# Optimization experiments

Measured on AMD Instinct MI355X. Metric: run time of the kernel, lower is better.

The kernel has to match this reference:

```python
import jax, jax.numpy as jnp
import numpy as np


def setup_inputs() -> dict:
    key = jax.random.key(0)
    kq, kk, kv = jax.random.split(key, 3)
    n, d = 8192, 128
    Q = jax.random.normal(kq, (n, d), dtype=jnp.float32)
    K = jax.random.normal(kk, (n, d), dtype=jnp.float32)
    V = jax.random.normal(kv, (n, d), dtype=jnp.float32)
    return {"Q": Q, "K": K, "V": V}


def reference(Q, K, V):
    # The blockwise online-softmax loops in the torch module compute exactly
    # softmax(Q @ K^T) @ V  -- note: NO 1/sqrt(d) scaling in the original.
    S = jnp.einsum('qd,kd->qk', Q, K)          # [n, n] scores
    P = jax.nn.softmax(S, axis=-1)             # numerically stable softmax
    O = jnp.einsum('qk,kd->qd', P, V)          # [n, d]
    return O
```

## Files before the change

kernel.cpp:

```cpp
#include <hip/hip_runtime.h>
#include <hip/hip_bf16.h>

#define N 8192
#define D 128
#define NSPLIT 8
#define KVSPLIT (N / NSPLIT)
#define KVBLK 64
#define NT (KVSPLIT / KVBLK)
#define L2E 1.442695041f

typedef __attribute__((ext_vector_type(8))) _Float16 half8;
typedef __attribute__((ext_vector_type(2))) __fp16 fp16x2;
typedef __attribute__((ext_vector_type(16))) float f32x16;

union H8 { fp16x2 h2[4]; half8 h8; };

__device__ __forceinline__ float fexp2(float x) {
    float r; asm("v_exp_f32 %0, %1" : "=v"(r) : "v"(x)); return r;
}

__global__ void prep_kernel(const float* __restrict__ Q, const float* __restrict__ K,
                            const float* __restrict__ V, _Float16* __restrict__ Qh,
                            _Float16* __restrict__ Kh, _Float16* __restrict__ Vtp) {
    __shared__ _Float16 tile[64][65];
    const int bid = blockIdx.x;
    const int tid = threadIdx.x;
    if (bid < 1024) {
        const float4* src = (const float4*)(bid < 512 ? Q : K);
        _Float16* dst = (bid < 512) ? Qh : Kh;
        const int b = bid & 511;
#pragma unroll
        for (int p = 0; p < 2; ++p) {
            int i = b * 512 + p * 256 + tid;
            float4 v = src[i];
            ushort4 o;
            o.x = __builtin_bit_cast(ushort, (_Float16)v.x);
            o.y = __builtin_bit_cast(ushort, (_Float16)v.y);
            o.z = __builtin_bit_cast(ushort, (_Float16)v.z);
            o.w = __builtin_bit_cast(ushort, (_Float16)v.w);
            *reinterpret_cast<ushort4*>(dst + (size_t)i * 4) = o;
        }
    } else {
        const int vbid = bid - 1024;
        const int k0 = (vbid & 127) * 64;
        const int d0 = (vbid >> 7) * 64;
#pragma unroll
        for (int p = 0; p < 16; ++p) {
            int flat = p * 256 + tid;
            int r = flat >> 6, cc = flat & 63;
            tile[r][cc] = (_Float16)(V[(size_t)(k0 + r) * D + d0 + cc]);
        }
        __syncthreads();
#pragma unroll
        for (int p = 0; p < 16; ++p) {
            int flat = p * 256 + tid;
            int dd = flat >> 6, kl = flat & 63;
            int kk = kl & 31;
            int s32 = 16 * (kk >> 4) + 8 * ((kk >> 2) & 1) + 4 * ((kk >> 3) & 1) + (kk & 3);
            Vtp[(size_t)(d0 + dd) * N + k0 + (kl & 32) + s32] = tile[kl][dd];
        }
    }
}

#define STAGE(kdst_, vdst_, kbase_)                                                   \
    {                                                                                 \
        _Pragma("unroll")                                                             \
        for (int p = 0; p < 4; ++p) {                                                 \
            int c4 = p * 256 + tid;                                                   \
            int row = c4 >> 4, chs = c4 & 15;                                         \
            int cc = (chs & 8) | ((chs & 7) ^ (row & 7));                             \
            __builtin_amdgcn_global_load_lds(                                         \
                (const __attribute__((address_space(1))) void*)(Kh + (size_t)((kbase_) + row) * D + cc * 8), \
                (__attribute__((address_space(3))) void*)((kdst_) + c4 * 8), 16, 0, 0);              \
        }                                                                             \
        _Pragma("unroll")                                                             \
        for (int p = 0; p < 4; ++p) {                                                 \
            int c4 = p * 256 + tid;                                                   \
            int dd = c4 >> 3, chs = c4 & 7;                                           \
            int cc = chs ^ (dd & 7);                                                  \
            __builtin_amdgcn_global_load_lds(                                         \
                (const __attribute__((address_space(1))) void*)(Vtp + (size_t)dd * N + (kbase_) + cc * 8),   \
                (__attribute__((address_space(3))) void*)((vdst_) + c4 * 8), 16, 0, 0);              \
        }                                                                             \
    }

__launch_bounds__(256, 2)
__global__ void fa_kernel(const _Float16* __restrict__ Qh, const _Float16* __restrict__ Kh,
                          const _Float16* __restrict__ Vtp, _Float16* __restrict__ Oph,
                          float* __restrict__ Mpart, float* __restrict__ Lpart) {
    __shared__ __align__(16) _Float16 smem[32768];

    const int tid  = threadIdx.x;
    const int w    = tid >> 6;
    const int lane = tid & 63;
    const int h    = lane >> 5;
    const int c    = lane & 31;
    const int bid  = blockIdx.x;
    const int split = bid & 7;
    const int bx   = bid >> 3;
    const int q0w  = bx * 128 + w * 32;
    const int kv0  = split * KVSPLIT;

    half8 qa[8];
    {
        const _Float16* qrow = Qh + (size_t)(q0w + c) * D + h * 8;
#pragma unroll
        for (int st = 0; st < 8; ++st)
            qa[st] = *reinterpret_cast<const half8*>(qrow + st * 16);
    }

    f32x16 oacc[4];
#pragma unroll
    for (int dt = 0; dt < 4; ++dt)
#pragma unroll
        for (int r = 0; r < 16; ++r) oacc[dt][r] = 0.f;
    float mrun = -1e30f, lrun = 0.f;
    H8 pk[4];

    STAGE(smem, smem + 16384, kv0);
    __syncthreads();

    for (int t = 0; t < NT; ++t) {
        const int cur = t & 1;
        if (t + 1 < NT)
            STAGE(smem + (cur ^ 1) * 8192, smem + 16384 + (cur ^ 1) * 8192,
                  kv0 + (t + 1) * KVBLK);

        const _Float16* kb = smem + cur * 8192;
        const _Float16* vb = smem + 16384 + cur * 8192;

        half8 kf[16];
#pragma unroll
        for (int st = 0; st < 8; ++st) {
            int ch = st * 2 + h;
            int pos = (ch & 8) | ((ch & 7) ^ (c & 7));
            kf[st]     = *reinterpret_cast<const half8*>(kb + c * 128 + pos * 8);
            kf[8 + st] = *reinterpret_cast<const half8*>(kb + (32 + c) * 128 + pos * 8);
        }

        f32x16 sb0, sb1;
#pragma unroll
        for (int r = 0; r < 16; ++r) { sb0[r] = 0.f; sb1[r] = 0.f; }
        __builtin_amdgcn_s_setprio(1);
#pragma unroll
        for (int st = 0; st < 8; ++st) {
            sb0 = __builtin_amdgcn_mfma_f32_32x32x16_f16(kf[st], qa[st], sb0, 0, 0, 0);
            sb1 = __builtin_amdgcn_mfma_f32_32x32x16_f16(kf[8 + st], qa[st], sb1, 0, 0, 0);
        }
        __builtin_amdgcn_s_setprio(0);

        float mx[16];
#pragma unroll
        for (int r = 0; r < 16; ++r) mx[r] = fmaxf(sb0[r], sb1[r]);
#pragma unroll
        for (int s = 8; s > 0; s >>= 1)
#pragma unroll
            for (int r = 0; r < s; ++r) mx[r] = fmaxf(mx[r], mx[r + s]);
        float pmax = fmaxf(mx[0], __shfl_xor(mx[0], 32));

        if (!__all(pmax <= mrun + 8.0f)) {
            float nm = fmaxf(mrun, pmax);
            float scl = fexp2((mrun - nm) * L2E);
            lrun *= scl;
#pragma unroll
            for (int dt = 0; dt < 4; ++dt)
#pragma unroll
                for (int r = 0; r < 16; ++r) oacc[dt][r] *= scl;
            mrun = nm;
        }
        const float nml = -mrun * L2E;
#pragma unroll
        for (int r = 0; r < 16; ++r) sb0[r] = fexp2(__builtin_fmaf(sb0[r], L2E, nml));
#pragma unroll
        for (int r = 0; r < 16; ++r) sb1[r] = fexp2(__builtin_fmaf(sb1[r], L2E, nml));
        float ts[16];
#pragma unroll
        for (int r = 0; r < 16; ++r) ts[r] = sb0[r] + sb1[r];
#pragma unroll
        for (int s = 8; s > 0; s >>= 1)
#pragma unroll
            for (int r = 0; r < s; ++r) ts[r] += ts[r + s];
        lrun += ts[0] + __shfl_xor(ts[0], 32);

#pragma unroll
        for (int i = 0; i < 4; ++i) {
            pk[0].h2[i] = __builtin_amdgcn_cvt_pkrtz(sb0[2 * i], sb0[2 * i + 1]);
            pk[1].h2[i] = __builtin_amdgcn_cvt_pkrtz(sb0[8 + 2 * i], sb0[8 + 2 * i + 1]);
            pk[2].h2[i] = __builtin_amdgcn_cvt_pkrtz(sb1[2 * i], sb1[2 * i + 1]);
            pk[3].h2[i] = __builtin_amdgcn_cvt_pkrtz(sb1[8 + 2 * i], sb1[8 + 2 * i + 1]);
        }

        half8 vf[16];
#pragma unroll
        for (int j = 0; j < 4; ++j) {
            int ch = j * 2 + h;
#pragma unroll
            for (int dt = 0; dt < 4; ++dt) {
                int dd = dt * 32 + c;
                int pos = ch ^ (dd & 7);
                vf[j * 4 + dt] = *reinterpret_cast<const half8*>(vb + dd * 64 + pos * 8);
            }
        }

        __builtin_amdgcn_s_setprio(1);
#pragma unroll
        for (int j = 0; j < 4; ++j)
#pragma unroll
            for (int dt = 0; dt < 4; ++dt)
                oacc[dt] = __builtin_amdgcn_mfma_f32_32x32x16_f16(vf[j * 4 + dt], pk[j].h8,
                                                                  oacc[dt], 0, 0, 0);
        __builtin_amdgcn_s_setprio(0);

        __syncthreads();
    }

    __syncthreads();
    float inv = 1.0f / lrun;
    float* epi = reinterpret_cast<float*>(smem) + w * 1088;
    const size_t sbase = (size_t)split * N;
#pragma unroll
    for (int dt = 0; dt < 4; ++dt) {
#pragma unroll
        for (int r = 0; r < 16; ++r) {
            int dloc = (r & 3) + 8 * (r >> 2) + 4 * h;
            epi[c * 33 + dloc] = oacc[dt][r] * inv;
        }
#pragma unroll
        for (int it = 0; it < 16; ++it) {
            int j = it * 64 + lane;
            int rr = j >> 5, cc2 = j & 31;
            Oph[(sbase + q0w + rr) * D + dt * 32 + cc2] = (_Float16)epi[rr * 33 + cc2];
        }
    }
    if (h == 0) {
        Mpart[sbase + q0w + c] = mrun;
        Lpart[sbase + q0w + c] = lrun;
    }
}

__global__ void fa_merge(const _Float16* __restrict__ Oph, const float* __restrict__ Mpart,
                         const float* __restrict__ Lpart, float* __restrict__ O) {
    int idx = blockIdx.x * 256 + threadIdx.x;
    int q = idx >> 7;
    int d = idx & 127;
    float m[NSPLIT];
    float M = -1e30f;
#pragma unroll
    for (int s = 0; s < NSPLIT; ++s) {
        m[s] = Mpart[s * N + q];
        M = fmaxf(M, m[s]);
    }
    float acc = 0.f, wsum = 0.f;
#pragma unroll
    for (int s = 0; s < NSPLIT; ++s) {
        float wgt = fexp2((m[s] - M) * L2E) * Lpart[s * N + q];
        acc += wgt * (float)Oph[((size_t)s * N + q) * D + d];
        wsum += wgt;
    }
    O[idx] = acc / wsum;
}

extern "C" void kernel_launch(void* const* d_in, const int* in_sizes, int n_in,
                              void* d_out, int out_size, void* d_ws, size_t ws_size,
                              hipStream_t stream) {
    const float* Q = (const float*)d_in[0];
    const float* K = (const float*)d_in[1];
    const float* V = (const float*)d_in[2];
    float* O = (float*)d_out;

    _Float16* Qh = (_Float16*)d_ws;
    _Float16* Kh = Qh + (size_t)N * D;
    _Float16* Vtp = Kh + (size_t)N * D;
    _Float16* Oph = Vtp + (size_t)N * D;
    float* Mpart = (float*)(Oph + (size_t)NSPLIT * N * D);
    float* Lpart = Mpart + (size_t)NSPLIT * N;

    hipLaunchKernelGGL(prep_kernel, dim3(1280), dim3(256), 0, stream,
                       Q, K, V, Qh, Kh, Vtp);
    hipLaunchKernelGGL(fa_kernel, dim3((N / 128) * NSPLIT), dim3(256), 0, stream,
                       Qh, Kh, Vtp, Oph, Mpart, Lpart);
    hipLaunchKernelGGL(fa_merge, dim3(N * D / 256), dim3(256), 0, stream,
                       Oph, Mpart, Lpart, O);
}
```

Baseline: 60.98 us.

## Process 64 query rows per wave and double KV splits

Each wave now handles two 32-row query tiles that share every K and V fragment read from LDS. This halves LDS traffic per MFMA and halves the KV tile loads per query. To keep the grid the same size, the KV range is split 16 ways instead of 8. The per-key-tile work is also split into two 32-key sub-steps with separate softmax updates. The cost is much higher register pressure (8 output accumulators plus two Q fragment sets), shorter KV loops per block, and twice the partial output written to and merged from workspace.

```diff
diff --git a/kernel.cpp b/kernel.cpp
--- a/kernel.cpp
+++ b/kernel.cpp
@@ -3,7 +3,7 @@
 
 #define N 8192
 #define D 128
-#define NSPLIT 8
+#define NSPLIT 16
 #define KVSPLIT (N / NSPLIT)
 #define KVBLK 64
 #define NT (KVSPLIT / KVBLK)
@@ -84,6 +84,44 @@
         }                                                                             \
     }
 
+#define SOFTMAX_PACK(S_, MR_, LR_, OB_, PK_)                                          \
+    {                                                                                 \
+        float mx[8];                                                                  \
+        _Pragma("unroll")                                                             \
+        for (int r = 0; r < 8; ++r) mx[r] = fmaxf(S_[r], S_[r + 8]);                  \
+        _Pragma("unroll")                                                             \
+        for (int sd = 4; sd > 0; sd >>= 1)                                            \
+            _Pragma("unroll")                                                         \
+            for (int r = 0; r < sd; ++r) mx[r] = fmaxf(mx[r], mx[r + sd]);            \
+        float pmax = fmaxf(mx[0], __shfl_xor(mx[0], 32));                             \
+        if (!__all(pmax <= MR_ + 8.0f)) {                                             \
+            float nm = fmaxf(MR_, pmax);                                              \
+            float scl = fexp2((MR_ - nm) * L2E);                                      \
+            LR_ *= scl;                                                               \
+            _Pragma("unroll")                                                         \
+            for (int dt = 0; dt < 4; ++dt)                                            \
+                _Pragma("unroll")                                                     \
+                for (int r = 0; r < 16; ++r) oacc[(OB_) + dt][r] *= scl;              \
+            MR_ = nm;                                                                 \
+        }                                                                             \
+        const float nml = -MR_ * L2E;                                                 \
+        _Pragma("unroll")                                                             \
+        for (int r = 0; r < 16; ++r) S_[r] = fexp2(__builtin_fmaf(S_[r], L2E, nml));  \
+        float tsum[8];                                                                \
+        _Pragma("unroll")                                                             \
+        for (int r = 0; r < 8; ++r) tsum[r] = S_[r] + S_[r + 8];                      \
+        _Pragma("unroll")                                                             \
+        for (int sd = 4; sd > 0; sd >>= 1)                                            \
+            _Pragma("unroll")                                                         \
+            for (int r = 0; r < sd; ++r) tsum[r] += tsum[r + sd];                     \
+        LR_ += tsum[0] + __shfl_xor(tsum[0], 32);                                     \
+        _Pragma("unroll")                                                             \
+        for (int i = 0; i < 4; ++i) {                                                 \
+            PK_[0].h2[i] = __builtin_amdgcn_cvt_pkrtz(S_[2 * i], S_[2 * i + 1]);      \
+            PK_[1].h2[i] = __builtin_amdgcn_cvt_pkrtz(S_[8 + 2 * i], S_[8 + 2 * i + 1]); \
+        }                                                                             \
+    }
+
 __launch_bounds__(256, 2)
 __global__ void fa_kernel(const _Float16* __restrict__ Qh, const _Float16* __restrict__ Kh,
                           const _Float16* __restrict__ Vtp, _Float16* __restrict__ Oph,
@@ -96,26 +134,28 @@
     const int h    = lane >> 5;
     const int c    = lane & 31;
     const int bid  = blockIdx.x;
-    const int split = bid & 7;
-    const int bx   = bid >> 3;
-    const int q0w  = bx * 128 + w * 32;
+    const int split = bid & (NSPLIT - 1);
+    const int bx   = bid >> 4;
+    const int q0w  = bx * 256 + w * 64;
     const int kv0  = split * KVSPLIT;
 
-    half8 qa[8];
+    half8 qaA[8], qaB[8];
     {
-        const _Float16* qrow = Qh + (size_t)(q0w + c) * D + h * 8;
-#pragma unroll
-        for (int st = 0; st < 8; ++st)
-            qa[st] = *reinterpret_cast<const half8*>(qrow + st * 16);
-    }
-
-    f32x16 oacc[4];
-#pragma unroll
-    for (int dt = 0; dt < 4; ++dt)
-#pragma unroll
-        for (int r = 0; r < 16; ++r) oacc[dt][r] = 0.f;
-    float mrun = -1e30f, lrun = 0.f;
-    H8 pk[4];
+        const _Float16* qrA = Qh + (size_t)(q0w + c) * D + h * 8;
+        const _Float16* qrB = Qh + (size_t)(q0w + 32 + c) * D + h * 8;
+#pragma unroll
+        for (int st = 0; st < 8; ++st) {
+            qaA[st] = *reinterpret_cast<const half8*>(qrA + st * 16);
+            qaB[st] = *reinterpret_cast<const half8*>(qrB + st * 16);
+        }
+    }
+
+    f32x16 oacc[8];
+#pragma unroll
+    for (int i = 0; i < 8; ++i)
+#pragma unroll
+        for (int r = 0; r < 16; ++r) oacc[i][r] = 0.f;
+    float mrunA = -1e30f, lrunA = 0.f, mrunB = -1e30f, lrunB = 0.f;
 
     STAGE(smem, smem + 16384, kv0);
     __syncthreads();
@@ -129,112 +169,87 @@
         const _Float16* kb = smem + cur * 8192;
         const _Float16* vb = smem + 16384 + cur * 8192;
 
-        half8 kf[16];
-#pragma unroll
-        for (int st = 0; st < 8; ++st) {
-            int ch = st * 2 + h;
-            int pos = (ch & 8) | ((ch & 7) ^ (c & 7));
-            kf[st]     = *reinterpret_cast<const half8*>(kb + c * 128 + pos * 8);
-            kf[8 + st] = *reinterpret_cast<const half8*>(kb + (32 + c) * 128 + pos * 8);
-        }
-
-        f32x16 sb0, sb1;
-#pragma unroll
-        for (int r = 0; r < 16; ++r) { sb0[r] = 0.f; sb1[r] = 0.f; }
-        __builtin_amdgcn_s_setprio(1);
-#pragma unroll
-        for (int st = 0; st < 8; ++st) {
-            sb0 = __builtin_amdgcn_mfma_f32_32x32x16_f16(kf[st], qa[st], sb0, 0, 0, 0);
-            sb1 = __builtin_amdgcn_mfma_f32_32x32x16_f16(kf[8 + st], qa[st], sb1, 0, 0, 0);
-        }
-        __builtin_amdgcn_s_setprio(0);
-
-        float mx[16];
-#pragma unroll
-        for (int r = 0; r < 16; ++r) mx[r] = fmaxf(sb0[r], sb1[r]);
-#pragma unroll
-        for (int s = 8; s > 0; s >>= 1)
-#pragma unroll
-            for (int r = 0; r < s; ++r) mx[r] = fmaxf(mx[r], mx[r + s]);
-        float pmax = fmaxf(mx[0], __shfl_xor(mx[0], 32));
-
-        if (!__all(pmax <= mrun + 8.0f)) {
-            float nm = fmaxf(mrun, pmax);
-            float scl = fexp2((mrun - nm) * L2E);
-            lrun *= scl;
-#pragma unroll
-            for (int dt = 0; dt < 4; ++dt)
-#pragma unroll
-                for (int r = 0; r < 16; ++r) oacc[dt][r] *= scl;
-            mrun = nm;
-        }
-        const float nml = -mrun * L2E;
-#pragma unroll
-        for (int r = 0; r < 16; ++r) sb0[r] = fexp2(__builtin_fmaf(sb0[r], L2E, nml));
-#pragma unroll
-        for (int r = 0; r < 16; ++r) sb1[r] = fexp2(__builtin_fmaf(sb1[r], L2E, nml));
-        float ts[16];
-#pragma unroll
-        for (int r = 0; r < 16; ++r) ts[r] = sb0[r] + sb1[r];
-#pragma unroll
-        for (int s = 8; s > 0; s >>= 1)
-#pragma unroll
-            for (int r = 0; r < s; ++r) ts[r] += ts[r + s];
-        lrun += ts[0] + __shfl_xor(ts[0], 32);
-
-#pragma unroll
-        for (int i = 0; i < 4; ++i) {
-            pk[0].h2[i] = __builtin_amdgcn_cvt_pkrtz(sb0[2 * i], sb0[2 * i + 1]);
-            pk[1].h2[i] = __builtin_amdgcn_cvt_pkrtz(sb0[8 + 2 * i], sb0[8 + 2 * i + 1]);
-            pk[2].h2[i] = __builtin_amdgcn_cvt_pkrtz(sb1[2 * i], sb1[2 * i + 1]);
-            pk[3].h2[i] = __builtin_amdgcn_cvt_pkrtz(sb1[8 + 2 * i], sb1[8 + 2 * i + 1]);
-        }
-
-        half8 vf[16];
-#pragma unroll
-        for (int j = 0; j < 4; ++j) {
-            int ch = j * 2 + h;
-#pragma unroll
-            for (int dt = 0; dt < 4; ++dt) {
-                int dd = dt * 32 + c;
-                int pos = ch ^ (dd & 7);
-                vf[j * 4 + dt] = *reinterpret_cast<const half8*>(vb + dd * 64 + pos * 8);
-            }
-        }
-
-        __builtin_amdgcn_s_setprio(1);
-#pragma unroll
-        for (int j = 0; j < 4; ++j)
-#pragma unroll
-            for (int dt = 0; dt < 4; ++dt)
-                oacc[dt] = __builtin_amdgcn_mfma_f32_32x32x16_f16(vf[j * 4 + dt], pk[j].h8,
-                                                                  oacc[dt], 0, 0, 0);
-        __builtin_amdgcn_s_setprio(0);
+#pragma unroll
+        for (int s = 0; s < 2; ++s) {
+            f32x16 sA, sB;
+#pragma unroll
+            for (int r = 0; r < 16; ++r) { sA[r] = 0.f; sB[r] = 0.f; }
+            __builtin_amdgcn_s_setprio(1);
+#pragma unroll
+            for (int st = 0; st < 8; ++st) {
+                int ch = st * 2 + h;
+                int pos = (ch & 8) | ((ch & 7) ^ (c & 7));
+                half8 kf = *reinterpret_cast<const half8*>(kb + (s * 32 + c) * 128 + pos * 8);
+                sA = __builtin_amdgcn_mfma_f32_32x32x16_f16(kf, qaA[st], sA, 0, 0, 0);
+                sB = __builtin_amdgcn_mfma_f32_32x32x16_f16(kf, qaB[st], sB, 0, 0, 0);
+            }
+            __builtin_amdgcn_s_setprio(0);
+
+            H8 pkA[2], pkB[2];
+            SOFTMAX_PACK(sA, mrunA, lrunA, 0, pkA)
+            SOFTMAX_PACK(sB, mrunB, lrunB, 4, pkB)
+
+            __builtin_amdgcn_s_setprio(1);
+#pragma unroll
+            for (int j = 0; j < 2; ++j) {
+                int ch = s * 4 + j * 2 + h;
+#pragma unroll
+                for (int dt = 0; dt < 4; ++dt) {
+                    int dd = dt * 32 + c;
+                    int pos = ch ^ (dd & 7);
+                    half8 vf = *reinterpret_cast<const half8*>(vb + dd * 64 + pos * 8);
+                    oacc[dt]     = __builtin_amdgcn_mfma_f32_32x32x16_f16(vf, pkA[j].h8, oacc[dt], 0, 0, 0);
+                    oacc[4 + dt] = __builtin_amdgcn_mfma_f32_32x32x16_f16(vf, pkB[j].h8, oacc[4 + dt], 0, 0, 0);
+                }
+            }
+            __builtin_amdgcn_s_setprio(0);
+        }
 
         __syncthreads();
     }
 
     __syncthreads();
-    float inv = 1.0f / lrun;
     float* epi = reinterpret_cast<float*>(smem) + w * 1088;
     const size_t sbase = (size_t)split * N;
-#pragma unroll
-    for (int dt = 0; dt < 4; ++dt) {
-#pragma unroll
-        for (int r = 0; r < 16; ++r) {
-            int dloc = (r & 3) + 8 * (r >> 2) + 4 * h;
-            epi[c * 33 + dloc] = oacc[dt][r] * inv;
-        }
-#pragma unroll
-        for (int it = 0; it < 16; ++it) {
-            int j = it * 64 + lane;
-            int rr = j >> 5, cc2 = j & 31;
-            Oph[(sbase + q0w + rr) * D + dt * 32 + cc2] = (_Float16)epi[rr * 33 + cc2];
+    {
+        float inv = 1.0f / lrunA;
+#pragma unroll
+        for (int dt = 0; dt < 4; ++dt) {
+#pragma unroll
+            for (int r = 0; r < 16; ++r) {
+                int dloc = (r & 3) + 8 * (r >> 2) + 4 * h;
+                epi[c * 33 + dloc] = oacc[dt][r] * inv;
+            }
+#pragma unroll
+            for (int it = 0; it < 16; ++it) {
+                int j = it * 64 + lane;
+                int rr = j >> 5, cc2 = j & 31;
+                Oph[(sbase + q0w + rr) * D + dt * 32 + cc2] = (_Float16)epi[rr * 33 + cc2];
+            }
+        }
+    }
+    {
+        float inv = 1.0f / lrunB;
+#pragma unroll
+        for (int dt = 0; dt < 4; ++dt) {
+#pragma unroll
+            for (int r = 0; r < 16; ++r) {
+                int dloc = (r & 3) + 8 * (r >> 2) + 4 * h;
+                epi[c * 33 + dloc] = oacc[4 + dt][r] * inv;
+            }
+#pragma unroll
+            for (int it = 0; it < 16; ++it) {
+                int j = it * 64 + lane;
+                int rr = j >> 5, cc2 = j & 31;
+                Oph[(sbase + q0w + 32 + rr) * D + dt * 32 + cc2] = (_Float16)epi[rr * 33 + cc2];
+            }
         }
     }
     if (h == 0) {
-        Mpart[sbase + q0w + c] = mrun;
-        Lpart[sbase + q0w + c] = lrun;
+        Mpart[sbase + q0w + c] = mrunA;
+        Lpart[sbase + q0w + c] = lrunA;
+        Mpart[sbase + q0w + 32 + c] = mrunB;
+        Lpart[sbase + q0w + 32 + c] = lrunB;
     }
 }
 
@@ -277,7 +292,7 @@
 
     hipLaunchKernelGGL(prep_kernel, dim3(1280), dim3(256), 0, stream,
                        Q, K, V, Qh, Kh, Vtp);
-    hipLaunchKernelGGL(fa_kernel, dim3((N / 128) * NSPLIT), dim3(256), 0, stream,
+    hipLaunchKernelGGL(fa_kernel, dim3((N / 256) * NSPLIT), dim3(256), 0, stream,
                        Qh, Kh, Vtp, Oph, Mpart, Lpart);
     hipLaunchKernelGGL(fa_merge, dim3(N * D / 256), dim3(256), 0, stream,
                        Oph, Mpart, Lpart, O);
```

New measurement: 87.09 us. 42.8% more time.

## Double KV splits, single-buffer LDS, and raise occupancy to four blocks per CU

Applied to the files above, without the earlier changes.

Splits the KV range into 16 chunks instead of 8 and drops the double-buffered LDS staging in favour of a single 32 KB buffer guarded by barriers. K and V fragments are now loaded just before each MFMA instead of being held in large register arrays. Together with launch bounds asking for 4 blocks per CU, this aims to raise occupancy so other waves hide memory latency. In exchange it loses the explicit prefetch overlap and doubles the partial-output traffic that the combine step must read and merge.

```diff
diff --git a/kernel.cpp b/kernel.cpp
--- a/kernel.cpp
+++ b/kernel.cpp
@@ -3,7 +3,7 @@
 
 #define N 8192
 #define D 128
-#define NSPLIT 8
+#define NSPLIT 16
 #define KVSPLIT (N / NSPLIT)
 #define KVBLK 64
 #define NT (KVSPLIT / KVBLK)
@@ -84,11 +84,11 @@
         }                                                                             \
     }
 
-__launch_bounds__(256, 2)
+__launch_bounds__(256, 4)
 __global__ void fa_kernel(const _Float16* __restrict__ Qh, const _Float16* __restrict__ Kh,
                           const _Float16* __restrict__ Vtp, _Float16* __restrict__ Oph,
                           float* __restrict__ Mpart, float* __restrict__ Lpart) {
-    __shared__ __align__(16) _Float16 smem[32768];
+    __shared__ __align__(16) _Float16 smem[16384];
 
     const int tid  = threadIdx.x;
     const int w    = tid >> 6;
@@ -96,10 +96,13 @@
     const int h    = lane >> 5;
     const int c    = lane & 31;
     const int bid  = blockIdx.x;
-    const int split = bid & 7;
-    const int bx   = bid >> 3;
+    const int split = bid & (NSPLIT - 1);
+    const int bx   = bid >> 4;
     const int q0w  = bx * 128 + w * 32;
     const int kv0  = split * KVSPLIT;
+
+    _Float16* const kb = smem;
+    _Float16* const vb = smem + 8192;
 
     half8 qa[8];
     {
@@ -117,35 +120,23 @@
     float mrun = -1e30f, lrun = 0.f;
     H8 pk[4];
 
-    STAGE(smem, smem + 16384, kv0);
-    __syncthreads();
-
     for (int t = 0; t < NT; ++t) {
-        const int cur = t & 1;
-        if (t + 1 < NT)
-            STAGE(smem + (cur ^ 1) * 8192, smem + 16384 + (cur ^ 1) * 8192,
-                  kv0 + (t + 1) * KVBLK);
-
-        const _Float16* kb = smem + cur * 8192;
-        const _Float16* vb = smem + 16384 + cur * 8192;
-
-        half8 kf[16];
+        if (t > 0) __syncthreads();
+        STAGE(kb, vb, kv0 + t * KVBLK);
+        __syncthreads();
+
+        f32x16 sb0, sb1;
+#pragma unroll
+        for (int r = 0; r < 16; ++r) { sb0[r] = 0.f; sb1[r] = 0.f; }
+        __builtin_amdgcn_s_setprio(1);
 #pragma unroll
         for (int st = 0; st < 8; ++st) {
             int ch = st * 2 + h;
             int pos = (ch & 8) | ((ch & 7) ^ (c & 7));
-            kf[st]     = *reinterpret_cast<const half8*>(kb + c * 128 + pos * 8);
-            kf[8 + st] = *reinterpret_cast<const half8*>(kb + (32 + c) * 128 + pos * 8);
-        }
-
-        f32x16 sb0, sb1;
-#pragma unroll
-        for (int r = 0; r < 16; ++r) { sb0[r] = 0.f; sb1[r] = 0.f; }
-        __builtin_amdgcn_s_setprio(1);
-#pragma unroll
-        for (int st = 0; st < 8; ++st) {
-            sb0 = __builtin_amdgcn_mfma_f32_32x32x16_f16(kf[st], qa[st], sb0, 0, 0, 0);
-            sb1 = __builtin_amdgcn_mfma_f32_32x32x16_f16(kf[8 + st], qa[st], sb1, 0, 0, 0);
+            half8 kf0 = *reinterpret_cast<const half8*>(kb + c * 128 + pos * 8);
+            half8 kf1 = *reinterpret_cast<const half8*>(kb + (32 + c) * 128 + pos * 8);
+            sb0 = __builtin_amdgcn_mfma_f32_32x32x16_f16(kf0, qa[st], sb0, 0, 0, 0);
+            sb1 = __builtin_amdgcn_mfma_f32_32x32x16_f16(kf1, qa[st], sb1, 0, 0, 0);
         }
         __builtin_amdgcn_s_setprio(0);
 
@@ -189,8 +180,7 @@
             pk[2].h2[i] = __builtin_amdgcn_cvt_pkrtz(sb1[2 * i], sb1[2 * i + 1]);
             pk[3].h2[i] = __builtin_amdgcn_cvt_pkrtz(sb1[8 + 2 * i], sb1[8 + 2 * i + 1]);
         }
-
-        half8 vf[16];
+        __builtin_amdgcn_s_setprio(1);
 #pragma unroll
         for (int j = 0; j < 4; ++j) {
             int ch = j * 2 + h;
@@ -198,20 +188,11 @@
             for (int dt = 0; dt < 4; ++dt) {
                 int dd = dt * 32 + c;
                 int pos = ch ^ (dd & 7);
-                vf[j * 4 + dt] = *reinterpret_cast<const half8*>(vb + dd * 64 + pos * 8);
+                half8 vf = *reinterpret_cast<const half8*>(vb + dd * 64 + pos * 8);
+                oacc[dt] = __builtin_amdgcn_mfma_f32_32x32x16_f16(vf, pk[j].h8, oacc[dt], 0, 0, 0);
             }
         }
-
-        __builtin_amdgcn_s_setprio(1);
-#pragma unroll
-        for (int j = 0; j < 4; ++j)
-#pragma unroll
-            for (int dt = 0; dt < 4; ++dt)
-                oacc[dt] = __builtin_amdgcn_mfma_f32_32x32x16_f16(vf[j * 4 + dt], pk[j].h8,
-                                                                  oacc[dt], 0, 0, 0);
         __builtin_amdgcn_s_setprio(0);
-
-        __syncthreads();
     }
 
     __syncthreads();
```

Result: slower. 116.7 us (+91.4%).
